# Optimization experiments

Hardware: AMD Instinct MI355X
Metric: run time of the kernel (lower is better)

## Reference

```python
import jax, jax.numpy as jnp
import numpy as np

B, N, HN, HE, H = 8, 128, 256, 128, 8
DH = HN // H
P = N * (N - 1) // 2


def _ln(x, g, b, eps=1e-5):
    m = jnp.mean(x, axis=-1, keepdims=True)
    v = jnp.mean((x - m) ** 2, axis=-1, keepdims=True)
    return (x - m) * jax.lax.rsqrt(v + eps) * g + b


def setup_inputs() -> dict:
    key = jax.random.key(0)
    ks = jax.random.split(key, 16)
    i1, i2 = np.triu_indices(N, k=1)  # all unordered pairs, P = N(N-1)/2
    s = lambda fan: 1.0 / np.sqrt(fan)
    return {
        "node_feat": jax.random.normal(ks[0], (B, N, HN), jnp.float32),
        "edge_feat": jax.random.normal(ks[1], (B, P, HE), jnp.float32),
        "x_idx1": jnp.asarray(i1, jnp.int32),
        "x_idx2": jnp.asarray(i2, jnp.int32),
        "mask_valid": jax.random.bernoulli(ks[2], 0.9, (B, P)).astype(jnp.float32),
        "Wqkv": jax.random.normal(ks[3], (HN, 3 * HN), jnp.float32) * s(HN),
        "bqkv": jnp.zeros((3 * HN,), jnp.float32),
        "Wev": jax.random.normal(ks[4], (HE, HN), jnp.float32) * s(HE),
        "bev": jnp.zeros((HN,), jnp.float32),
        "Wea": jax.random.normal(ks[5], (HE, H), jnp.float32) * s(HE),
        "bea": jnp.zeros((H,), jnp.float32),
        "Wo": jax.random.normal(ks[6], (2 * HN, HN), jnp.float32) * s(2 * HN),
        "bo": jnp.zeros((HN,), jnp.float32),
        "Wsk": jax.random.normal(ks[7], (HN, 2 * HN), jnp.float32) * s(HN),
        "bsk": jnp.zeros((2 * HN,), jnp.float32),
        "gn": jnp.ones((HN,), jnp.float32),
        "bn": jnp.zeros((HN,), jnp.float32),
        "ge": jnp.ones((HE,), jnp.float32),
        "be": jnp.zeros((HE,), jnp.float32),
    }


def reference(node_feat, edge_feat, x_idx1, x_idx2, mask_valid,
              Wqkv, bqkv, Wev, bev, Wea, bea, Wo, bo, Wsk, bsk,
              gn, bn, ge, be):
    n_in = _ln(node_feat, gn, bn)                      # [B,N,HN]
    e_in = _ln(edge_feat, ge, be)                      # [B,P,HE]
    q, k, v = jnp.split(n_in @ Wqkv + bqkv, 3, axis=-1)
    to_h = lambda t: t.reshape(B, -1, H, DH).transpose(0, 2, 1, 3)
    q, k, v = to_h(q), to_h(k), to_h(v)                # [B,H,N,DH]
    e_val = to_h(e_in @ Wev + bev)                     # [B,H,P,DH]
    e_adj = (e_in @ Wea + bea).transpose(0, 2, 1)      # [B,H,P]

    scale = DH ** -0.5
    logits = jnp.einsum('bhqd,bhkd->bhqk', q, k) * scale  # [B,H,N,N]
    # per-pair logits; torch stacks [qk, edge_adj] then sums -> just add
    l_node1 = logits[:, :, x_idx1, x_idx2] + e_adj     # node i1 attends to i2
    l_node2 = logits[:, :, x_idx2, x_idx1] + e_adj     # node i2 attends to i1
    v_node1 = e_val + v[:, :, x_idx2]                  # value node i1 receives
    v_node2 = e_val + v[:, :, x_idx1]

    # group the 2P directed edges by destination node (= torch cat+sort+reshape)
    cat_idx = jnp.concatenate([x_idx1, x_idx2])        # [2P]
    order = jnp.argsort(cat_idx)                       # stable sort
    gl = jnp.concatenate([l_node1, l_node2], axis=2)[:, :, order].reshape(B, H, N, N - 1)
    gv = jnp.concatenate([v_node1, v_node2], axis=2)[:, :, order].reshape(B, H, N, N - 1, DH)
    gm = jnp.concatenate([mask_valid, mask_valid], axis=1)[:, order].reshape(B, N, N - 1)[:, None]  # [B,1,N,N-1]

    gl = jnp.where(gm == 0.0, -9e15, gl)
    probs = jax.nn.softmax(gl, axis=3)
    probs = probs * jnp.any(gm != 0.0, axis=3, keepdims=True).astype(probs.dtype)
    attn = jnp.einsum('bhnk,bhnkd->bhnd', probs, gv)   # [B,H,N,DH]
    attn = attn.transpose(0, 2, 1, 3).reshape(B, N, HN)

    comb = jax.nn.gelu(jnp.concatenate([n_in, attn], axis=-1) @ Wo + bo, approximate=False)
    val, gate = jnp.split(comb @ Wsk + bsk, 2, axis=-1)
    g = jax.nn.sigmoid(gate)
    return node_feat * (1.0 - g) + val * g
```

## Files before the change

### kernel.cpp

```cpp
#include <hip/hip_runtime.h>
#include <hip/hip_bf16.h>
#include <math.h>

#define BB 8
#define NN 128
#define HN 256
#define HE 128
#define NH 8
#define DH 32
#define PP 8128
#define BP (BB*PP)

typedef __hip_bfloat16 bf16;
typedef __attribute__((ext_vector_type(8))) short bf16x8;

__device__ __forceinline__ float bf2f(bf16 x){ return __bfloat162float(x); }
__device__ __forceinline__ float bfraw2f(short u){
  return __uint_as_float(((unsigned)(unsigned short)u) << 16);
}

__device__ __forceinline__ float wave_sum(float v){
  #pragma unroll
  for (int off=32; off>=1; off>>=1) v += __shfl_xor(v, off, 64);
  return v;
}
__device__ __forceinline__ float g16_sum(float v){
  #pragma unroll
  for (int off=8; off>=1; off>>=1) v += __shfl_xor(v, off, 16);
  return v;
}

__device__ __forceinline__ int pair_idx(int a, int c){
  int i = a < c ? a : c;
  int j = a < c ? c : a;
  return ((i*(255 - i))>>1) + (j - i - 1);
}

#define C_NODE 0LL
#define C_MASK 262144LL
#define C_WQKV 327168LL
#define C_BQKV 523776LL
#define C_WEV  524544LL
#define C_BEV  557312LL
#define C_WEA  557568LL
#define C_BEA  558592LL
#define C_WO   558600LL
#define C_BO   689672LL
#define C_WSK  689928LL
#define C_BSK  821000LL
#define C_GN   821512LL
#define C_BN   821768LL
#define C_GE   822024LL
#define C_BE   822152LL
#define IOFF   822400LL
#define TOT8   102785
#define CONVBLKS 402
#define I_NIN  0LL
#define I_Q    262144LL
#define I_K    524288LL
#define I_V    786432LL
#define I_EA2  1572864LL
#define I_XG   2093056LL
#define I_WT   14577664LL
#define I_WOB  14594048LL
#define I_WSKB 14659584LL
#define I_FLG  14725120LL

struct SrcPtrs { const void* p[16]; };

__global__ __launch_bounds__(256) void k_convert(SrcPtrs sp, float* __restrict__ dst,
                                                 int* __restrict__ flags,
                                                 const unsigned short* __restrict__ nodeRaw,
                                                 const void* __restrict__ rawWev,
                                                 bf16* __restrict__ Wt,
                                                 const void* __restrict__ rawWo,
                                                 const void* __restrict__ rawWsk,
                                                 bf16* __restrict__ WoB,
                                                 bf16* __restrict__ WskB)
{
  __shared__ int sbad;
  if (threadIdx.x == 0) sbad = 0;
  __syncthreads();
  {
    int bad = 0;
    for (int i = threadIdx.x; i < 1024; i += 256){
      unsigned e = (nodeRaw[i] >> 7) & 0xFFu;
      if (e >= 194u) bad = 1;
    }
    if (bad) sbad = 1;
  }
  __syncthreads();
  const int f32 = sbad;
  if (blockIdx.x == 0 && threadIdx.x == 0) flags[0] = f32;

  if (blockIdx.x >= CONVBLKS + 128){
    int o = (blockIdx.x - (CONVBLKS + 128))*256 + threadIdx.x;
    const void* src = (o < 16384) ? rawWo : rawWsk;
    bf16* dw = (o < 16384) ? WoB : WskB;
    int lo = (o < 16384) ? o : o - 16384;
    if (f32){
      const float4* s4 = (const float4*)src;
      float4 a0 = s4[2*lo], a1 = s4[2*lo+1];
      union { float4 f; bf16 h[8]; } cv;
      cv.h[0]=__float2bfloat16(a0.x); cv.h[1]=__float2bfloat16(a0.y);
      cv.h[2]=__float2bfloat16(a0.z); cv.h[3]=__float2bfloat16(a0.w);
      cv.h[4]=__float2bfloat16(a1.x); cv.h[5]=__float2bfloat16(a1.y);
      cv.h[6]=__float2bfloat16(a1.z); cv.h[7]=__float2bfloat16(a1.w);
      *reinterpret_cast<float4*>(dw + lo*8) = cv.f;
    } else {
      *reinterpret_cast<float4*>(dw + lo*8) = ((const float4*)src)[lo];
    }
    return;
  }

  if (blockIdx.x >= CONVBLKS){
    int idx = (blockIdx.x - CONVBLKS)*256 + threadIdx.x;
    float v = f32 ? ((const float*)rawWev)[idx]
                  : bfraw2f(((const short*)rawWev)[idx]);
    Wt[(idx & 255)*128 + (idx >> 8)] = __float2bfloat16(v);
    return;
  }

  int o = blockIdx.x*256 + threadIdx.x;
  if (o >= TOT8) return;
  const int cum[17] = {0,32768,40896,65472,65568,69664,69696,69824,69825,
                       86209,86241,102625,102689,102721,102753,102769,102785};
  int s = 0;
  #pragma unroll
  for (int i = 1; i <= 15; i++) if (o >= cum[i]) s = i;
  const int li = o - cum[s];
  float4 r0, r1;
  if (f32){
    const float4* src = (const float4*)sp.p[s];
    r0 = src[2*li]; r1 = src[2*li+1];
  } else {
    union { float4 f; unsigned short u[8]; } cv;
    cv.f = ((const float4*)sp.p[s])[li];
    r0.x = __uint_as_float((unsigned)cv.u[0] << 16);
    r0.y = __uint_as_float((unsigned)cv.u[1] << 16);
    r0.z = __uint_as_float((unsigned)cv.u[2] << 16);
    r0.w = __uint_as_float((unsigned)cv.u[3] << 16);
    r1.x = __uint_as_float((unsigned)cv.u[4] << 16);
    r1.y = __uint_as_float((unsigned)cv.u[5] << 16);
    r1.z = __uint_as_float((unsigned)cv.u[6] << 16);
    r1.w = __uint_as_float((unsigned)cv.u[7] << 16);
  }
  float4* d = (float4*)(dst + (long long)cum[s]*8);
  d[2*li]   = r0;
  d[2*li+1] = r1;
}

__global__ __launch_bounds__(256) void k1_node_ln_qkv(
    const float* __restrict__ cnode, const float* __restrict__ cWqkv,
    const float* __restrict__ cbqkv, const float* __restrict__ cgn, const float* __restrict__ cbn,
    float* __restrict__ nin_ws, float* __restrict__ q_ws, float* __restrict__ k_ws,
    float* __restrict__ v_ws)
{
  __shared__ float xln[4][HN];
  const int t = threadIdx.x, wv = t>>6, lane = t&63;
  const int cb = blockIdx.x % 3;
  const int g0 = (blockIdx.x / 3) * 4;
  {
    int g = g0 + wv;
    float x[4];
    #pragma unroll
    for (int i=0;i<4;i++) x[i] = cnode[g*HN + lane + 64*i];
    float s = x[0]+x[1]+x[2]+x[3];
    s = wave_sum(s);
    float m = s * (1.0f/HN);
    float q = 0.f;
    #pragma unroll
    for (int i=0;i<4;i++){ float d = x[i]-m; q += d*d; }
    q = wave_sum(q);
    float rstd = rsqrtf(fmaxf(q*(1.0f/HN), 0.f) + 1e-5f);
    #pragma unroll
    for (int i=0;i<4;i++){
      int c = lane + 64*i;
      float y = (x[i]-m)*rstd*cgn[c] + cbn[c];
      xln[wv][c] = y;
      if (cb == 0) nin_ws[g*HN + c] = y;
    }
  }
  __syncthreads();
  const int col = cb*256 + t;
  float acc[4];
  {
    float bb = cbqkv[col];
    #pragma unroll
    for (int r=0;r<4;r++) acc[r] = bb;
  }
  for (int k=0;k<HN;k+=4){
    float4 xv[4];
    #pragma unroll
    for (int r=0;r<4;r++) xv[r] = *reinterpret_cast<const float4*>(&xln[r][k]);
    #pragma unroll
    for (int kk=0;kk<4;kk++){
      float w = cWqkv[(k+kk)*768 + col];
      #pragma unroll
      for (int r=0;r<4;r++) acc[r] = fmaf((&xv[r].x)[kk], w, acc[r]);
    }
  }
  if (cb == 2){
    #pragma unroll
    for (int r=0;r<4;r++) v_ws[(long)(g0+r)*HN + t] = acc[r];
  } else {
    float* dstp = (cb == 0) ? q_ws : k_ws;
    const int h = t>>5, d = t&31;
    #pragma unroll
    for (int r=0;r<4;r++){
      int g = g0 + r;
      int b = g>>7, n = g&127;
      dstp[((b*NH + h)*NN + n)*DH + d] = acc[r];
    }
  }
}

__global__ __launch_bounds__(256) void k2a_edge_ln(
    const void* __restrict__ edge_raw, const float* __restrict__ cWea,
    const float* __restrict__ cbea, const float* __restrict__ cge,
    const float* __restrict__ cbe, const float* __restrict__ cmask,
    bf16* __restrict__ xg, float* __restrict__ ea2, const int* __restrict__ flags)
{
  __shared__ float xlnS[16][136];
  __shared__ float part[128];
  const int t = threadIdx.x;
  const int R0 = blockIdx.x*16;
  const int b = R0 / PP;
  const int p0 = R0 - b*PP;
  const int f32 = flags[0];
  {
    int r = t>>4, sub = t&15;
    long base = (long)(R0 + r)*HE + sub*8;
    float x[8];
    if (f32){
      const float* cef = (const float*)edge_raw + base;
      float4 a0 = *reinterpret_cast<const float4*>(cef);
      float4 a1 = *reinterpret_cast<const float4*>(cef + 4);
      x[0]=a0.x; x[1]=a0.y; x[2]=a0.z; x[3]=a0.w;
      x[4]=a1.x; x[5]=a1.y; x[6]=a1.z; x[7]=a1.w;
    } else {
      union { float4 f; short u[8]; } cv;
      cv.f = *reinterpret_cast<const float4*>((const bf16*)edge_raw + base);
      #pragma unroll
      for (int i=0;i<8;i++) x[i] = bfraw2f(cv.u[i]);
    }
    float s = 0.f;
    #pragma unroll
    for (int i=0;i<8;i++) s += x[i];
    s = g16_sum(s);
    float m = s*(1.0f/HE);
    float q = 0.f;
    #pragma unroll
    for (int i=0;i<8;i++){ float dd = x[i]-m; q += dd*dd; }
    q = g16_sum(q);
    float rstd = rsqrtf(fmaxf(q*(1.0f/HE), 0.f) + 1e-5f);
    float y[8];
    #pragma unroll
    for (int i=0;i<8;i++){
      int c = sub*8 + i;
      y[i] = (x[i]-m)*rstd*cge[c] + cbe[c];
    }
    float4 y0; y0.x=y[0]; y0.y=y[1]; y0.z=y[2]; y0.w=y[3];
    float4 y1; y1.x=y[4]; y1.y=y[5]; y1.z=y[6]; y1.w=y[7];
    *reinterpret_cast<float4*>(&xlnS[r][sub*8])     = y0;
    *reinterpret_cast<float4*>(&xlnS[r][sub*8 + 4]) = y1;
  }
  __syncthreads();
  {
    int r = t>>4, c0 = (t&15)*8;
    union { float4 f; bf16 h[8]; } o;
    #pragma unroll
    for (int i=0;i<8;i++) o.h[i] = __float2bfloat16(xlnS[r][c0+i]);
    *reinterpret_cast<float4*>(xg + (long)(R0 + r)*HE + c0) = o.f;
  }
  {
    const int c = t & 7, r = (t>>3) & 15, half = t>>7;
    const int pid = r*8 + c;
    float s = half ? 0.0f : cbea[c];
    const int k0 = half*64;
    #pragma unroll 8
    for (int k=k0; k<k0+64; k++) s = fmaf(xlnS[r][k], cWea[k*NH + c], s);
    if (half){ part[pid] = s; }
    __syncthreads();
    if (!half){
      s += part[pid];
      int p = p0 + r;
      float mk = cmask[b*PP + p];
      ea2[((long)b*PP + p)*8 + c] = (mk != 0.0f) ? s : -9e15f;
    }
  }
}

__global__ __launch_bounds__(256, 4) void k345(
    const float* __restrict__ q_ws,
    const float* __restrict__ k_ws,
    const float* __restrict__ v_ws,
    const bf16* __restrict__ xg,
    const float* __restrict__ ea2,
    const bf16* __restrict__ Wt,
    const float* __restrict__ cbev,
    const float* __restrict__ nin_ws,
    const bf16* __restrict__ WoB,
    const float* __restrict__ cbo,
    const bf16* __restrict__ WskB,
    const float* __restrict__ cbsk,
    const float* __restrict__ cnode,
    void* __restrict__ out, const int* __restrict__ flags)
{
  __shared__ __align__(16) bf16  xgS[128][128];
  __shared__ __align__(16) float sS[8][128];
  float* xc    = (float*)xgS;
  float* combS = xc + 512;
  float* psE   = xc + 768;
  float* psG   = xc + 768 + 2048;
  const int t = threadIdx.x;
  const int bid = blockIdx.x;
  const int swz = (bid & 7)*128 + (bid >> 3);
  const int n = swz & 127, b = swz >> 7;
  const int g = b*NN + n;
  const int h = t >> 5, ln = t & 31;

  float4 qv[8];
  const float* qb = q_ws + (((long)b*NH + h)*NN + n)*DH;
  #pragma unroll
  for (int d4=0; d4<8; d4++) qv[d4] = *reinterpret_cast<const float4*>(qb + d4*4);
  float eav[4];
  const float* eab = ea2 + (long)b*PP*8;
  #pragma unroll
  for (int j=0;j<4;j++){
    int m = ln + 32*j;
    int ms = (m == n) ? (m ^ 1) : m;
    eav[j] = eab[(long)pair_idx(n, ms)*8 + h];
  }
  const bf16* xgb = xg + (long)b*PP*HE;
  const int rowb = t >> 4, seg = t & 15;
  float4 xr[8];
  #pragma unroll
  for (int it=0; it<8; ++it){
    int row = it*16 + rowb;
    int ms = (row == n) ? (row ^ 1) : row;
    int pr = pair_idx(n, ms);
    xr[it] = *reinterpret_cast<const float4*>(xgb + (long)pr*HE + seg*8);
  }

  const float scale = 0.17677669529663687f;
  const float* kb = k_ws + ((long)b*NH + h)*NN*DH;
  float l[4];
  float mx = -INFINITY;
  int valid = 0;
  #pragma unroll
  for (int j=0;j<4;j++){
    int m = ln + 32*j;
    const float* kr = kb + m*DH;
    float dot = 0.f;
    #pragma unroll
    for (int d4=0; d4<8; d4++){
      float4 kv = *reinterpret_cast<const float4*>(kr + d4*4);
      dot = fmaf(qv[d4].x, kv.x, dot);
      dot = fmaf(qv[d4].y, kv.y, dot);
      dot = fmaf(qv[d4].z, kv.z, dot);
      dot = fmaf(qv[d4].w, kv.w, dot);
    }
    bool self = (m == n);
    l[j] = self ? -INFINITY : fmaf(dot, scale, eav[j]);
    if (!self && eav[j] > -8.9e15f) valid = 1;
    mx = fmaxf(mx, l[j]);
  }
  #pragma unroll
  for (int off=16; off>=1; off>>=1) mx = fmaxf(mx, __shfl_xor(mx, off, 32));
  float e[4], s = 0.f;
  #pragma unroll
  for (int j=0;j<4;j++){ e[j] = __expf(l[j]-mx); s += e[j]; }
  float av = valid ? 1.f : 0.f;
  #pragma unroll
  for (int off=16; off>=1; off>>=1){
    s  += __shfl_xor(s,  off, 32);
    av += __shfl_xor(av, off, 32);
  }
  float inv = (av > 0.f) ? (1.0f/s) : 0.f;
  float pj0 = e[0]*inv, pj1 = e[1]*inv, pj2 = e[2]*inv, pj3 = e[3]*inv;

  #pragma unroll
  for (int it=0; it<8; ++it){
    int row = it*16 + rowb;
    *reinterpret_cast<float4*>(&xgS[row][seg*8]) = xr[it];
  }
  __syncthreads();

  const float* vb = v_ws + (long)b*NN*HN + h*DH + ln;
  float S0=0.f,S1=0.f,S2=0.f,S3=0.f,T=0.f;
  #pragma unroll
  for (int j=0;j<4;j++){
    float pcur = (j==0) ? pj0 : (j==1) ? pj1 : (j==2) ? pj2 : pj3;
    #pragma unroll 2
    for (int mm=0; mm<32; mm+=4){
      #pragma unroll
      for (int i=0;i<4;i++){
        int m = j*32 + mm + i;
        float pm = __shfl(pcur, mm + i, 32);
        short4 xv = *reinterpret_cast<const short4*>(&xgS[m][ln*4]);
        S0 = fmaf(pm, bfraw2f(xv.x), S0);
        S1 = fmaf(pm, bfraw2f(xv.y), S1);
        S2 = fmaf(pm, bfraw2f(xv.z), S2);
        S3 = fmaf(pm, bfraw2f(xv.w), S3);
        T  = fmaf(pm, vb[m*HN], T);
      }
    }
  }
  {
    float4 sv; sv.x=S0; sv.y=S1; sv.z=S2; sv.w=S3;
    *reinterpret_cast<float4*>(&sS[h][ln*4]) = sv;
  }
  __syncthreads();

  float nin_v = nin_ws[(long)g*HN + t];
  float acc = T + ((av > 0.f) ? cbev[t] : 0.f);
  const bf16* wr = Wt + t*HE;
  #pragma unroll 4
  for (int k0=0;k0<128;k0+=8){
    float4 sa = *reinterpret_cast<const float4*>(&sS[h][k0]);
    float4 sb = *reinterpret_cast<const float4*>(&sS[h][k0+4]);
    bf16x8 wv = *reinterpret_cast<const bf16x8*>(wr + k0);
    acc = fmaf(sa.x, bfraw2f(wv[0]), acc);
    acc = fmaf(sa.y, bfraw2f(wv[1]), acc);
    acc = fmaf(sa.z, bfraw2f(wv[2]), acc);
    acc = fmaf(sa.w, bfraw2f(wv[3]), acc);
    acc = fmaf(sb.x, bfraw2f(wv[4]), acc);
    acc = fmaf(sb.y, bfraw2f(wv[5]), acc);
    acc = fmaf(sb.z, bfraw2f(wv[6]), acc);
    acc = fmaf(sb.w, bfraw2f(wv[7]), acc);
  }
  xc[t]       = nin_v;
  xc[256 + t] = acc;
  __syncthreads();

  {
    const int c8 = t & 31, ks = t >> 5;
    const int cbase = c8*8;
    float a8[8];
    #pragma unroll
    for (int i=0;i<8;i++) a8[i] = 0.f;
    const bf16* wp = WoB + (long)(ks*64)*HN + cbase;
    #pragma unroll 8
    for (int kk=0; kk<64; ++kk){
      float xk = xc[ks*64 + kk];
      bf16x8 w8 = *reinterpret_cast<const bf16x8*>(wp);
      wp += HN;
      a8[0] = fmaf(xk, bfraw2f(w8[0]), a8[0]);
      a8[1] = fmaf(xk, bfraw2f(w8[1]), a8[1]);
      a8[2] = fmaf(xk, bfraw2f(w8[2]), a8[2]);
      a8[3] = fmaf(xk, bfraw2f(w8[3]), a8[3]);
      a8[4] = fmaf(xk, bfraw2f(w8[4]), a8[4]);
      a8[5] = fmaf(xk, bfraw2f(w8[5]), a8[5]);
      a8[6] = fmaf(xk, bfraw2f(w8[6]), a8[6]);
      a8[7] = fmaf(xk, bfraw2f(w8[7]), a8[7]);
    }
    #pragma unroll
    for (int i=0;i<8;i++) psE[ks*256 + c8 + 32*i] = a8[i];
  }
  __syncthreads();
  {
    int idx = (t>>3) + 32*(t&7);
    float co = cbo[t];
    #pragma unroll
    for (int ks=0; ks<8; ++ks) co += psE[ks*256 + idx];
    co = 0.5f*co*(1.0f + erff(co*0.7071067811865475f));
    combS[t] = co;
  }
  __syncthreads();

  {
    const int c8 = t & 31, ks = t >> 5;
    const int cbase = c8*8;
    float av8[8], ag8[8];
    #pragma unroll
    for (int i=0;i<8;i++){ av8[i] = 0.f; ag8[i] = 0.f; }
    const bf16* wvp = WskB + (long)(ks*32)*512 + cbase;
    const bf16* wgp = wvp + 256;
    #pragma unroll 4
    for (int kk=0; kk<32; ++kk){
      float cx = combS[ks*32 + kk];
      bf16x8 wv8 = *reinterpret_cast<const bf16x8*>(wvp);
      bf16x8 wg8 = *reinterpret_cast<const bf16x8*>(wgp);
      wvp += 512; wgp += 512;
      av8[0] = fmaf(cx, bfraw2f(wv8[0]), av8[0]);
      av8[1] = fmaf(cx, bfraw2f(wv8[1]), av8[1]);
      av8[2] = fmaf(cx, bfraw2f(wv8[2]), av8[2]);
      av8[3] = fmaf(cx, bfraw2f(wv8[3]), av8[3]);
      av8[4] = fmaf(cx, bfraw2f(wv8[4]), av8[4]);
      av8[5] = fmaf(cx, bfraw2f(wv8[5]), av8[5]);
      av8[6] = fmaf(cx, bfraw2f(wv8[6]), av8[6]);
      av8[7] = fmaf(cx, bfraw2f(wv8[7]), av8[7]);
      ag8[0] = fmaf(cx, bfraw2f(wg8[0]), ag8[0]);
      ag8[1] = fmaf(cx, bfraw2f(wg8[1]), ag8[1]);
      ag8[2] = fmaf(cx, bfraw2f(wg8[2]), ag8[2]);
      ag8[3] = fmaf(cx, bfraw2f(wg8[3]), ag8[3]);
      ag8[4] = fmaf(cx, bfraw2f(wg8[4]), ag8[4]);
      ag8[5] = fmaf(cx, bfraw2f(wg8[5]), ag8[5]);
      ag8[6] = fmaf(cx, bfraw2f(wg8[6]), ag8[6]);
      ag8[7] = fmaf(cx, bfraw2f(wg8[7]), ag8[7]);
    }
    #pragma unroll
    for (int i=0;i<8;i++){
      psE[ks*256 + c8 + 32*i] = av8[i];
      psG[ks*256 + c8 + 32*i] = ag8[i];
    }
  }
  __syncthreads();
  {
    int idx = (t>>3) + 32*(t&7);
    float av5 = cbsk[t], ag5 = cbsk[t+256];
    #pragma unroll
    for (int ks=0; ks<8; ++ks){
      av5 += psE[ks*256 + idx];
      ag5 += psG[ks*256 + idx];
    }
    float gg = 1.0f/(1.0f + __expf(-ag5));
    long idxg = (long)g*HN + t;
    float nf = cnode[idxg];
    float res = nf*(1.0f - gg) + av5*gg;
    if (flags[0]) ((float*)out)[idxg] = res;
    else ((bf16*)out)[idxg] = __float2bfloat16(res);
  }
}

extern "C" void kernel_launch(void* const* d_in, const int* in_sizes, int n_inputs,
                              void* d_out, int out_size, void* d_ws, size_t ws_size,
                              hipStream_t stream)
{
  float* ws = (float*)d_ws;
  float* c_node = ws + C_NODE;
  float* c_mask = ws + C_MASK;
  float* c_Wqkv = ws + C_WQKV;
  float* c_bqkv = ws + C_BQKV;
  float* c_bev  = ws + C_BEV;
  float* c_Wea  = ws + C_WEA;
  float* c_bea  = ws + C_BEA;
  float* c_bo   = ws + C_BO;
  float* c_bsk  = ws + C_BSK;
  float* c_gn   = ws + C_GN;
  float* c_bn   = ws + C_BN;
  float* c_ge   = ws + C_GE;
  float* c_be   = ws + C_BE;
  float* base   = ws + IOFF;
  float* nin_ws  = base + I_NIN;
  float* q_ws    = base + I_Q;
  float* k_ws    = base + I_K;
  float* v_ws    = base + I_V;
  float* ea2_ws  = base + I_EA2;
  bf16*  xg_ws   = (bf16*)(base + I_XG);
  bf16*  wt_ws   = (bf16*)(base + I_WT);
  bf16*  wob_ws  = (bf16*)(base + I_WOB);
  bf16*  wskb_ws = (bf16*)(base + I_WSKB);
  int*   flags   = (int*)(base + I_FLG);

  SrcPtrs sp;
  sp.p[0]  = d_in[0];
  sp.p[1]  = d_in[4];
  sp.p[2]  = d_in[5];
  sp.p[3]  = d_in[6];
  sp.p[4]  = d_in[7];
  sp.p[5]  = d_in[8];
  sp.p[6]  = d_in[9];
  sp.p[7]  = d_in[10];
  sp.p[8]  = d_in[11];
  sp.p[9]  = d_in[12];
  sp.p[10] = d_in[13];
  sp.p[11] = d_in[14];
  sp.p[12] = d_in[15];
  sp.p[13] = d_in[16];
  sp.p[14] = d_in[17];
  sp.p[15] = d_in[18];

  k_convert<<<CONVBLKS + 256, 256, 0, stream>>>(sp, ws, flags,
                                                (const unsigned short*)d_in[0],
                                                d_in[7], wt_ws,
                                                d_in[11], d_in[13],
                                                wob_ws, wskb_ws);
  k1_node_ln_qkv<<<768, 256, 0, stream>>>(c_node, c_Wqkv, c_bqkv, c_gn, c_bn,
                                          nin_ws, q_ws, k_ws, v_ws);
  k2a_edge_ln<<<BP/16, 256, 0, stream>>>(d_in[1], c_Wea, c_bea, c_ge, c_be, c_mask,
                                         xg_ws, ea2_ws, flags);
  k345<<<BB*NN, 256, 0, stream>>>(q_ws, k_ws, v_ws, xg_ws, ea2_ws, wt_ws, c_bev,
                                  nin_ws, wob_ws, c_bo, wskb_ws, c_bsk,
                                  c_node, d_out, flags);
}
```

Baseline: 190.4 us.

## Remove separate convert kernel; read raw inputs directly and fold weight prep into edge kernel

```diff
diff --git a/kernel.cpp b/kernel.cpp
--- a/kernel.cpp
+++ b/kernel.cpp
@@ -36,25 +36,28 @@
   return ((i*(255 - i))>>1) + (j - i - 1);
 }
 
-#define C_NODE 0LL
-#define C_MASK 262144LL
-#define C_WQKV 327168LL
-#define C_BQKV 523776LL
-#define C_WEV  524544LL
+__device__ __forceinline__ int detect_f32(const unsigned short* nodeRaw, int* sbad){
+  if (threadIdx.x == 0) *sbad = 0;
+  __syncthreads();
+  ushort4 v = reinterpret_cast<const ushort4*>(nodeRaw)[threadIdx.x];
+  int bad = 0;
+  if (((v.x >> 7) & 0xFFu) >= 194u) bad = 1;
+  if (((v.y >> 7) & 0xFFu) >= 194u) bad = 1;
+  if (((v.z >> 7) & 0xFFu) >= 194u) bad = 1;
+  if (((v.w >> 7) & 0xFFu) >= 194u) bad = 1;
+  if (bad) *sbad = 1;
+  __syncthreads();
+  return *sbad;
+}
+
+__device__ __forceinline__ float dualf(const void* p, long i, int f32){
+  return f32 ? ((const float*)p)[i] : bfraw2f(((const short*)p)[i]);
+}
+
 #define C_BEV  557312LL
-#define C_WEA  557568LL
-#define C_BEA  558592LL
-#define C_WO   558600LL
 #define C_BO   689672LL
-#define C_WSK  689928LL
 #define C_BSK  821000LL
-#define C_GN   821512LL
-#define C_BN   821768LL
-#define C_GE   822024LL
-#define C_BE   822152LL
 #define IOFF   822400LL
-#define TOT8   102785
-#define CONVBLKS 402
 #define I_NIN  0LL
 #define I_Q    262144LL
 #define I_K    524288LL
@@ -64,107 +67,35 @@
 #define I_WT   14577664LL
 #define I_WOB  14594048LL
 #define I_WSKB 14659584LL
-#define I_FLG  14725120LL
-
-struct SrcPtrs { const void* p[16]; };
-
-__global__ __launch_bounds__(256) void k_convert(SrcPtrs sp, float* __restrict__ dst,
-                                                 int* __restrict__ flags,
-                                                 const unsigned short* __restrict__ nodeRaw,
-                                                 const void* __restrict__ rawWev,
-                                                 bf16* __restrict__ Wt,
-                                                 const void* __restrict__ rawWo,
-                                                 const void* __restrict__ rawWsk,
-                                                 bf16* __restrict__ WoB,
-                                                 bf16* __restrict__ WskB)
-{
-  __shared__ int sbad;
-  if (threadIdx.x == 0) sbad = 0;
-  __syncthreads();
-  {
-    int bad = 0;
-    for (int i = threadIdx.x; i < 1024; i += 256){
-      unsigned e = (nodeRaw[i] >> 7) & 0xFFu;
-      if (e >= 194u) bad = 1;
-    }
-    if (bad) sbad = 1;
-  }
-  __syncthreads();
-  const int f32 = sbad;
-  if (blockIdx.x == 0 && threadIdx.x == 0) flags[0] = f32;
-
-  if (blockIdx.x >= CONVBLKS + 128){
-    int o = (blockIdx.x - (CONVBLKS + 128))*256 + threadIdx.x;
-    const void* src = (o < 16384) ? rawWo : rawWsk;
-    bf16* dw = (o < 16384) ? WoB : WskB;
-    int lo = (o < 16384) ? o : o - 16384;
-    if (f32){
-      const float4* s4 = (const float4*)src;
-      float4 a0 = s4[2*lo], a1 = s4[2*lo+1];
-      union { float4 f; bf16 h[8]; } cv;
-      cv.h[0]=__float2bfloat16(a0.x); cv.h[1]=__float2bfloat16(a0.y);
-      cv.h[2]=__float2bfloat16(a0.z); cv.h[3]=__float2bfloat16(a0.w);
-      cv.h[4]=__float2bfloat16(a1.x); cv.h[5]=__float2bfloat16(a1.y);
-      cv.h[6]=__float2bfloat16(a1.z); cv.h[7]=__float2bfloat16(a1.w);
-      *reinterpret_cast<float4*>(dw + lo*8) = cv.f;
-    } else {
-      *reinterpret_cast<float4*>(dw + lo*8) = ((const float4*)src)[lo];
-    }
-    return;
-  }
-
-  if (blockIdx.x >= CONVBLKS){
-    int idx = (blockIdx.x - CONVBLKS)*256 + threadIdx.x;
-    float v = f32 ? ((const float*)rawWev)[idx]
-                  : bfraw2f(((const short*)rawWev)[idx]);
-    Wt[(idx & 255)*128 + (idx >> 8)] = __float2bfloat16(v);
-    return;
-  }
-
-  int o = blockIdx.x*256 + threadIdx.x;
-  if (o >= TOT8) return;
-  const int cum[17] = {0,32768,40896,65472,65568,69664,69696,69824,69825,
-                       86209,86241,102625,102689,102721,102753,102769,102785};
-  int s = 0;
-  #pragma unroll
-  for (int i = 1; i <= 15; i++) if (o >= cum[i]) s = i;
-  const int li = o - cum[s];
-  float4 r0, r1;
-  if (f32){
-    const float4* src = (const float4*)sp.p[s];
-    r0 = src[2*li]; r1 = src[2*li+1];
-  } else {
-    union { float4 f; unsigned short u[8]; } cv;
-    cv.f = ((const float4*)sp.p[s])[li];
-    r0.x = __uint_as_float((unsigned)cv.u[0] << 16);
-    r0.y = __uint_as_float((unsigned)cv.u[1] << 16);
-    r0.z = __uint_as_float((unsigned)cv.u[2] << 16);
-    r0.w = __uint_as_float((unsigned)cv.u[3] << 16);
-    r1.x = __uint_as_float((unsigned)cv.u[4] << 16);
-    r1.y = __uint_as_float((unsigned)cv.u[5] << 16);
-    r1.z = __uint_as_float((unsigned)cv.u[6] << 16);
-    r1.w = __uint_as_float((unsigned)cv.u[7] << 16);
-  }
-  float4* d = (float4*)(dst + (long long)cum[s]*8);
-  d[2*li]   = r0;
-  d[2*li+1] = r1;
-}
+
+#define EDGEBLKS 4064
+#define PREPBLKS 257
 
 __global__ __launch_bounds__(256) void k1_node_ln_qkv(
-    const float* __restrict__ cnode, const float* __restrict__ cWqkv,
-    const float* __restrict__ cbqkv, const float* __restrict__ cgn, const float* __restrict__ cbn,
+    const void* __restrict__ nodeRaw, const void* __restrict__ WqkvRaw,
+    const void* __restrict__ bqkvRaw, const void* __restrict__ gnRaw,
+    const void* __restrict__ bnRaw,
     float* __restrict__ nin_ws, float* __restrict__ q_ws, float* __restrict__ k_ws,
     float* __restrict__ v_ws)
 {
   __shared__ float xln[4][HN];
+  __shared__ int sbad;
   const int t = threadIdx.x, wv = t>>6, lane = t&63;
+  const int f32 = detect_f32((const unsigned short*)nodeRaw, &sbad);
   const int cb = blockIdx.x % 3;
   const int g0 = (blockIdx.x / 3) * 4;
   {
     int g = g0 + wv;
     float x[4];
-    #pragma unroll
-    for (int i=0;i<4;i++) x[i] = cnode[g*HN + lane + 64*i];
+    if (f32){
+      const float* cn = (const float*)nodeRaw;
+      #pragma unroll
+      for (int i=0;i<4;i++) x[i] = cn[(long)g*HN + lane + 64*i];
+    } else {
+      const short* cn = (const short*)nodeRaw;
+      #pragma unroll
+      for (int i=0;i<4;i++) x[i] = bfraw2f(cn[(long)g*HN + lane + 64*i]);
+    }
     float s = x[0]+x[1]+x[2]+x[3];
     s = wave_sum(s);
     float m = s * (1.0f/HN);
@@ -176,28 +107,44 @@
     #pragma unroll
     for (int i=0;i<4;i++){
       int c = lane + 64*i;
-      float y = (x[i]-m)*rstd*cgn[c] + cbn[c];
+      float y = (x[i]-m)*rstd*dualf(gnRaw, c, f32) + dualf(bnRaw, c, f32);
       xln[wv][c] = y;
-      if (cb == 0) nin_ws[g*HN + c] = y;
+      if (cb == 0) nin_ws[(long)g*HN + c] = y;
     }
   }
   __syncthreads();
   const int col = cb*256 + t;
   float acc[4];
   {
-    float bb = cbqkv[col];
+    float bb = dualf(bqkvRaw, col, f32);
     #pragma unroll
     for (int r=0;r<4;r++) acc[r] = bb;
   }
-  for (int k=0;k<HN;k+=4){
-    float4 xv[4];
-    #pragma unroll
-    for (int r=0;r<4;r++) xv[r] = *reinterpret_cast<const float4*>(&xln[r][k]);
-    #pragma unroll
-    for (int kk=0;kk<4;kk++){
-      float w = cWqkv[(k+kk)*768 + col];
-      #pragma unroll
-      for (int r=0;r<4;r++) acc[r] = fmaf((&xv[r].x)[kk], w, acc[r]);
+  if (f32){
+    const float* W = (const float*)WqkvRaw;
+    for (int k=0;k<HN;k+=4){
+      float4 xv[4];
+      #pragma unroll
+      for (int r=0;r<4;r++) xv[r] = *reinterpret_cast<const float4*>(&xln[r][k]);
+      #pragma unroll
+      for (int kk=0;kk<4;kk++){
+        float w = W[(long)(k+kk)*768 + col];
+        #pragma unroll
+        for (int r=0;r<4;r++) acc[r] = fmaf((&xv[r].x)[kk], w, acc[r]);
+      }
+    }
+  } else {
+    const short* W = (const short*)WqkvRaw;
+    for (int k=0;k<HN;k+=4){
+      float4 xv[4];
+      #pragma unroll
+      for (int r=0;r<4;r++) xv[r] = *reinterpret_cast<const float4*>(&xln[r][k]);
+      #pragma unroll
+      for (int kk=0;kk<4;kk++){
+        float w = bfraw2f(W[(long)(k+kk)*768 + col]);
+        #pragma unroll
+        for (int r=0;r<4;r++) acc[r] = fmaf((&xv[r].x)[kk], w, acc[r]);
+      }
     }
   }
   if (cb == 2){
@@ -216,18 +163,61 @@
 }
 
 __global__ __launch_bounds__(256) void k2a_edge_ln(
-    const void* __restrict__ edge_raw, const float* __restrict__ cWea,
-    const float* __restrict__ cbea, const float* __restrict__ cge,
-    const float* __restrict__ cbe, const float* __restrict__ cmask,
-    bf16* __restrict__ xg, float* __restrict__ ea2, const int* __restrict__ flags)
+    const void* __restrict__ edge_raw, const void* __restrict__ WeaRaw,
+    const void* __restrict__ beaRaw, const void* __restrict__ geRaw,
+    const void* __restrict__ beRaw, const void* __restrict__ maskRaw,
+    const void* __restrict__ nodeRaw,
+    const void* __restrict__ WevRaw, const void* __restrict__ bevRaw,
+    const void* __restrict__ WoRaw, const void* __restrict__ boRaw,
+    const void* __restrict__ WskRaw, const void* __restrict__ bskRaw,
+    bf16* __restrict__ xg, float* __restrict__ ea2,
+    bf16* __restrict__ Wt, bf16* __restrict__ WoB, bf16* __restrict__ WskB,
+    float* __restrict__ ws)
 {
   __shared__ float xlnS[16][136];
   __shared__ float part[128];
+  __shared__ int sbad;
   const int t = threadIdx.x;
+  const int f32 = detect_f32((const unsigned short*)nodeRaw, &sbad);
+
+  if (blockIdx.x >= EDGEBLKS){
+    const int pb = blockIdx.x - EDGEBLKS;
+    if (pb < 128){
+      int idx = pb*256 + t;
+      float v = dualf(WevRaw, idx, f32);
+      Wt[(idx & 255)*128 + (idx >> 8)] = __float2bfloat16(v);
+    } else if (pb < 256){
+      int o = (pb-128)*256 + t;
+      const void* src = (o < 16384) ? WoRaw : WskRaw;
+      bf16* dw = (o < 16384) ? WoB : WskB;
+      int lo = (o < 16384) ? o : o - 16384;
+      if (f32){
+        const float4* s4 = (const float4*)src;
+        float4 a0 = s4[2*lo], a1 = s4[2*lo+1];
+        union { float4 f; bf16 h[8]; } cv;
+        cv.h[0]=__float2bfloat16(a0.x); cv.h[1]=__float2bfloat16(a0.y);
+        cv.h[2]=__float2bfloat16(a0.z); cv.h[3]=__float2bfloat16(a0.w);
+        cv.h[4]=__float2bfloat16(a1.x); cv.h[5]=__float2bfloat16(a1.y);
+        cv.h[6]=__float2bfloat16(a1.z); cv.h[7]=__float2bfloat16(a1.w);
+        *reinterpret_cast<float4*>(dw + lo*8) = cv.f;
+      } else {
+        *reinterpret_cast<float4*>(dw + lo*8) = ((const float4*)src)[lo];
+      }
+    } else {
+      for (int i = t; i < 1024; i += 256){
+        const void* src; float* dst; int li;
+        if (i < 256){ src = bevRaw; dst = ws + C_BEV; li = i; }
+        else if (i < 512){ src = boRaw; dst = ws + C_BO; li = i-256; }
+        else { src = bskRaw; dst = ws + C_BSK; li = i-512; }
+        dst[li] = dualf(src, li, f32);
+      }
+    }
+    return;
+  }
+
   const int R0 = blockIdx.x*16;
   const int b = R0 / PP;
   const int p0 = R0 - b*PP;
-  const int f32 = flags[0];
   {
     int r = t>>4, sub = t&15;
     long base = (long)(R0 + r)*HE + sub*8;
@@ -258,7 +248,7 @@
     #pragma unroll
     for (int i=0;i<8;i++){
       int c = sub*8 + i;
-      y[i] = (x[i]-m)*rstd*cge[c] + cbe[c];
+      y[i] = (x[i]-m)*rstd*dualf(geRaw, c, f32) + dualf(beRaw, c, f32);
     }
     float4 y0; y0.x=y[0]; y0.y=y[1]; y0.z=y[2]; y0.w=y[3];
     float4 y1; y1.x=y[4]; y1.y=y[5]; y1.z=y[6]; y1.w=y[7];
@@ -276,16 +266,17 @@
   {
     const int c = t & 7, r = (t>>3) & 15, half = t>>7;
     const int pid = r*8 + c;
-    float s = half ? 0.0f : cbea[c];
+    float s = half ? 0.0f : dualf(beaRaw, c, f32);
     const int k0 = half*64;
     #pragma unroll 8
-    for (int k=k0; k<k0+64; k++) s = fmaf(xlnS[r][k], cWea[k*NH + c], s);
+    for (int k=k0; k<k0+64; k++)
+      s = fmaf(xlnS[r][k], dualf(WeaRaw, k*NH + c, f32), s);
     if (half){ part[pid] = s; }
     __syncthreads();
     if (!half){
       s += part[pid];
       int p = p0 + r;
-      float mk = cmask[b*PP + p];
+      float mk = dualf(maskRaw, (long)b*PP + p, f32);
       ea2[((long)b*PP + p)*8 + c] = (mk != 0.0f) ? s : -9e15f;
     }
   }
@@ -304,17 +295,19 @@
     const float* __restrict__ cbo,
     const bf16* __restrict__ WskB,
     const float* __restrict__ cbsk,
-    const float* __restrict__ cnode,
-    void* __restrict__ out, const int* __restrict__ flags)
+    const void* __restrict__ nodeRaw,
+    void* __restrict__ out)
 {
   __shared__ __align__(16) bf16  xgS[128][128];
   __shared__ __align__(16) float sS[8][128];
+  __shared__ int sbad;
   float* xc    = (float*)xgS;
   float* combS = xc + 512;
   float* psE   = xc + 768;
   float* psG   = xc + 768 + 2048;
   const int t = threadIdx.x;
   const int bid = blockIdx.x;
+  const int f32 = detect_f32((const unsigned short*)nodeRaw, &sbad);
   const int swz = (bid & 7)*128 + (bid >> 3);
   const int n = swz & 127, b = swz >> 7;
   const int g = b*NN + n;
@@ -517,9 +510,9 @@
     }
     float gg = 1.0f/(1.0f + __expf(-ag5));
     long idxg = (long)g*HN + t;
-    float nf = cnode[idxg];
+    float nf = dualf(nodeRaw, idxg, f32);
     float res = nf*(1.0f - gg) + av5*gg;
-    if (flags[0]) ((float*)out)[idxg] = res;
+    if (f32) ((float*)out)[idxg] = res;
     else ((bf16*)out)[idxg] = __float2bfloat16(res);
   }
 }
@@ -529,19 +522,6 @@
                               hipStream_t stream)
 {
   float* ws = (float*)d_ws;
-  float* c_node = ws + C_NODE;
-  float* c_mask = ws + C_MASK;
-  float* c_Wqkv = ws + C_WQKV;
-  float* c_bqkv = ws + C_BQKV;
-  float* c_bev  = ws + C_BEV;
-  float* c_Wea  = ws + C_WEA;
-  float* c_bea  = ws + C_BEA;
-  float* c_bo   = ws + C_BO;
-  float* c_bsk  = ws + C_BSK;
-  float* c_gn   = ws + C_GN;
-  float* c_bn   = ws + C_BN;
-  float* c_ge   = ws + C_GE;
-  float* c_be   = ws + C_BE;
   float* base   = ws + IOFF;
   float* nin_ws  = base + I_NIN;
   float* q_ws    = base + I_Q;
@@ -552,36 +532,14 @@
   bf16*  wt_ws   = (bf16*)(base + I_WT);
   bf16*  wob_ws  = (bf16*)(base + I_WOB);
   bf16*  wskb_ws = (bf16*)(base + I_WSKB);
-  int*   flags   = (int*)(base + I_FLG);
-
-  SrcPtrs sp;
-  sp.p[0]  = d_in[0];
-  sp.p[1]  = d_in[4];
-  sp.p[2]  = d_in[5];
-  sp.p[3]  = d_in[6];
-  sp.p[4]  = d_in[7];
-  sp.p[5]  = d_in[8];
-  sp.p[6]  = d_in[9];
-  sp.p[7]  = d_in[10];
-  sp.p[8]  = d_in[11];
-  sp.p[9]  = d_in[12];
-  sp.p[10] = d_in[13];
-  sp.p[11] = d_in[14];
-  sp.p[12] = d_in[15];
-  sp.p[13] = d_in[16];
-  sp.p[14] = d_in[17];
-  sp.p[15] = d_in[18];
-
-  k_convert<<<CONVBLKS + 256, 256, 0, stream>>>(sp, ws, flags,
-                                                (const unsigned short*)d_in[0],
-                                                d_in[7], wt_ws,
-                                                d_in[11], d_in[13],
-                                                wob_ws, wskb_ws);
-  k1_node_ln_qkv<<<768, 256, 0, stream>>>(c_node, c_Wqkv, c_bqkv, c_gn, c_bn,
-                                          nin_ws, q_ws, k_ws, v_ws);
-  k2a_edge_ln<<<BP/16, 256, 0, stream>>>(d_in[1], c_Wea, c_bea, c_ge, c_be, c_mask,
-                                         xg_ws, ea2_ws, flags);
-  k345<<<BB*NN, 256, 0, stream>>>(q_ws, k_ws, v_ws, xg_ws, ea2_ws, wt_ws, c_bev,
-                                  nin_ws, wob_ws, c_bo, wskb_ws, c_bsk,
-                                  c_node, d_out, flags);
-}
+
+  k1_node_ln_qkv<<<768, 256, 0, stream>>>(d_in[0], d_in[5], d_in[6], d_in[15],
+                                          d_in[16], nin_ws, q_ws, k_ws, v_ws);
+  k2a_edge_ln<<<EDGEBLKS + PREPBLKS, 256, 0, stream>>>(
+      d_in[1], d_in[9], d_in[10], d_in[17], d_in[18], d_in[4], d_in[0],
+      d_in[7], d_in[8], d_in[11], d_in[12], d_in[13], d_in[14],
+      xg_ws, ea2_ws, wt_ws, wob_ws, wskb_ws, ws);
+  k345<<<BB*NN, 256, 0, stream>>>(q_ws, k_ws, v_ws, xg_ws, ea2_ws, wt_ws,
+                                  ws + C_BEV, nin_ws, wob_ws, ws + C_BO,
+                                  wskb_ws, ws + C_BSK, d_in[0], d_out);
+}
```

Result: slower. 215.1 us (+13.0%).
